# Kernel optimization log

Measured on AMD Instinct MI355X. Metric: run time of the kernel, lower is better.

## Reference

```python
import jax, jax.numpy as jnp
import numpy as np

INPUT, HIDDEN = 8, 16

def setup_inputs() -> dict:
    key = jax.random.key(0)
    ks = jax.random.split(key, 7)
    s_ih = 1.0 / np.sqrt(HIDDEN)
    x = jax.random.normal(ks[0], (8192, 512, INPUT), dtype=jnp.float32)
    W_ih = jax.random.uniform(ks[1], (HIDDEN, INPUT), jnp.float32, -s_ih, s_ih)
    W_hh = jax.random.uniform(ks[2], (HIDDEN, HIDDEN), jnp.float32, -s_ih, s_ih)
    b_ih = jax.random.uniform(ks[3], (HIDDEN,), jnp.float32, -s_ih, s_ih)
    b_hh = jax.random.uniform(ks[4], (HIDDEN,), jnp.float32, -s_ih, s_ih)
    s_fc = 1.0 / np.sqrt(HIDDEN)
    fc_w = jax.random.uniform(ks[5], (1, HIDDEN), jnp.float32, -s_fc, s_fc)
    fc_b = jax.random.uniform(ks[6], (1,), jnp.float32, -s_fc, s_fc)
    return {"x": x, "W_ih": W_ih, "W_hh": W_hh, "b_ih": b_ih, "b_hh": b_hh, "fc_w": fc_w, "fc_b": fc_b}

def reference(x, W_ih, W_hh, b_ih, b_hh, fc_w, fc_b):
    B, T, _ = x.shape
    # Precompute input projection for all timesteps: [B, T, H]
    xp = jnp.einsum('bti,hi->bth', x, W_ih) + b_ih + b_hh
    h0 = jnp.zeros((B, HIDDEN), dtype=x.dtype)

    def step(h, xt):
        h_new = jnp.tanh(xt + h @ W_hh.T)
        return h_new, None

    h_last, _ = jax.lax.scan(step, h0, jnp.swapaxes(xp, 0, 1))
    return h_last @ fc_w.T + fc_b  # [B, 1]
```

## Files before the change

kernel.cpp:

```cpp
#include <hip/hip_runtime.h>
#include <stdint.h>


#define RNN_B   8192
#define RNN_T   512
#define RNN_IN  8
#define RNN_H   16
#define TC      32
#define NE      4
#define XROW    260
#define NTILE   (RNN_T / TC)
#define BUFSZ   (NE * XROW)

#if defined(__has_builtin)
#if __has_builtin(__builtin_amdgcn_mov_dpp)
#define ROR16(x, N) ((uint32_t)__builtin_amdgcn_mov_dpp((int)(x), 0x120 + (N), 0xF, 0xF, false))
#endif
#endif
#ifndef ROR16
#define ROR16(x, N) ((uint32_t)__builtin_amdgcn_update_dpp(0, (int)(x), 0x120 + (N), 0xF, 0xF, false))
#endif

__device__ __forceinline__ void gather16(uint32_t in, uint32_t v[16]) {
    v[0]  = in;
    v[8]  = ROR16(v[0], 8);
    v[4]  = ROR16(v[0], 4);
    v[12] = ROR16(v[8], 4);
    v[2]  = ROR16(v[0], 2);
    v[6]  = ROR16(v[4], 2);
    v[10] = ROR16(v[8], 2);
    v[14] = ROR16(v[12], 2);
    v[1]  = ROR16(v[0], 1);
    v[3]  = ROR16(v[2], 1);
    v[5]  = ROR16(v[4], 1);
    v[7]  = ROR16(v[6], 1);
    v[9]  = ROR16(v[8], 1);
    v[11] = ROR16(v[10], 1);
    v[13] = ROR16(v[12], 1);
    v[15] = ROR16(v[14], 1);
}

static __device__ __forceinline__ void stage(const float* __restrict__ x,
                                             float* lds_base, int b0, int t0,
                                             int lane)
{
#pragma unroll
    for (int e = 0; e < NE; ++e) {
        const float* gp = x + ((size_t)(b0 + e) * RNN_T + t0) * RNN_IN + lane * 4;
        float* lp = lds_base + e * XROW;
        __builtin_amdgcn_global_load_lds(
            (const __attribute__((address_space(1))) uint32_t*)gp,
            (__attribute__((address_space(3))) uint32_t*)lp,
            16, 0, 0);
    }
}

__global__ __launch_bounds__(64) void rnn_valu_kernel(
    const float* __restrict__ x,
    const float* __restrict__ W_ih,
    const float* __restrict__ W_hh,
    const float* __restrict__ b_ih,
    const float* __restrict__ b_hh,
    const float* __restrict__ fc_w,
    const float* __restrict__ fc_b,
    float* __restrict__ out)
{
    __shared__ __align__(16) float xs[2 * BUFSZ];

    const int lane = (int)threadIdx.x;
    const int j    = lane & 15;
    const int g    = lane >> 4;
    const int b0   = (int)blockIdx.x * NE;
    const float C2 = 2.8853900817779268f;

    uint32_t sv[16];
    gather16((uint32_t)j, sv);

    float whh[RNN_H];
    float rsum = 0.0f;
#pragma unroll
    for (int m = 0; m < 16; ++m) {
        const float w = W_hh[j * RNN_H + (int)sv[m]];
        whh[m] = -2.0f * C2 * w;
        rsum  += w;
    }
    const float bias_l = C2 * (b_ih[j] + b_hh[j]) + C2 * rsum;

    float wih[RNN_IN];
#pragma unroll
    for (int i = 0; i < RNN_IN; i += 4) {
        const float4 w = *(const float4*)(W_ih + j * RNN_IN + i);
        wih[i] = C2 * w.x; wih[i+1] = C2 * w.y; wih[i+2] = C2 * w.z; wih[i+3] = C2 * w.w;
    }

    stage(x, xs, b0, 0, lane);
    __syncthreads();

    float rv = 0.5f;

    for (int tile = 0; tile < NTILE; ++tile) {
        const int cur = tile & 1;

        const float* xg = xs + cur * BUFSZ + g * XROW;
        float xp[TC];
#pragma unroll
        for (int tt = 0; tt < TC; ++tt) {
            const float4 xa = *(const float4*)(xg + tt * 8);
            const float4 xb = *(const float4*)(xg + tt * 8 + 4);
            float t0 = fmaf(wih[0], xa.x, bias_l);
            t0 = fmaf(wih[1], xa.y, t0);
            t0 = fmaf(wih[2], xa.z, t0);
            t0 = fmaf(wih[3], xa.w, t0);
            float t1 = wih[4] * xb.x;
            t1 = fmaf(wih[5], xb.y, t1);
            t1 = fmaf(wih[6], xb.z, t1);
            t1 = fmaf(wih[7], xb.w, t1);
            xp[tt] = t0 + t1;
        }

        if (tile + 1 < NTILE)
            stage(x, xs + (cur ^ 1) * BUFSZ, b0, (tile + 1) * TC, lane);

#pragma unroll
        for (int tt = 0; tt < TC; ++tt) {
            uint32_t v[16];
            gather16(__float_as_uint(rv), v);

            float c0 = fmaf(whh[0],  __uint_as_float(v[0]),  xp[tt]);
            c0 = fmaf(whh[8],  __uint_as_float(v[8]),  c0);
            c0 = fmaf(whh[4],  __uint_as_float(v[4]),  c0);
            c0 = fmaf(whh[2],  __uint_as_float(v[2]),  c0);

            float c1 = whh[12] * __uint_as_float(v[12]);
            c1 = fmaf(whh[6],  __uint_as_float(v[6]),  c1);
            c1 = fmaf(whh[10], __uint_as_float(v[10]), c1);
            c1 = fmaf(whh[14], __uint_as_float(v[14]), c1);

            float c2 = whh[1] * __uint_as_float(v[1]);
            c2 = fmaf(whh[3],  __uint_as_float(v[3]),  c2);
            c2 = fmaf(whh[5],  __uint_as_float(v[5]),  c2);
            c2 = fmaf(whh[7],  __uint_as_float(v[7]),  c2);

            float c3 = whh[9] * __uint_as_float(v[9]);
            c3 = fmaf(whh[11], __uint_as_float(v[11]), c3);
            c3 = fmaf(whh[13], __uint_as_float(v[13]), c3);
            c3 = fmaf(whh[15], __uint_as_float(v[15]), c3);

            const float s = (c0 + c1) + (c2 + c3);

            const float e = __builtin_amdgcn_exp2f(s);
            rv = __builtin_amdgcn_rcpf(e + 1.0f);
        }
        __syncthreads();
    }

    const float h = fmaf(-2.0f, rv, 1.0f);
    float vsum = h * fc_w[j];
    vsum += __shfl_xor(vsum, 1);
    vsum += __shfl_xor(vsum, 2);
    vsum += __shfl_xor(vsum, 4);
    vsum += __shfl_xor(vsum, 8);
    if (j == 0) out[b0 + g] = vsum + fc_b[0];
}

extern "C" void kernel_launch(void* const* d_in, const int* in_sizes, int n_in,
                              void* d_out, int out_size, void* d_ws, size_t ws_size,
                              hipStream_t stream)
{
    const float* x    = (const float*)d_in[0];
    const float* W_ih = (const float*)d_in[1];
    const float* W_hh = (const float*)d_in[2];
    const float* b_ih = (const float*)d_in[3];
    const float* b_hh = (const float*)d_in[4];
    const float* fc_w = (const float*)d_in[5];
    const float* fc_b = (const float*)d_in[6];
    float* out = (float*)d_out;

    dim3 grid(RNN_B / NE);
    dim3 block(64);
    rnn_valu_kernel<<<grid, block, 0, stream>>>(x, W_ih, W_hh, b_ih, b_hh, fc_w, fc_b, out);
}
```

Measured before the change: 256.8 us.

## Use packed fp16 dot2 with split hi/lo weights for recurrent matvec

Packs the recurrent state into fp16 pairs and computes the 16-term hidden matvec with v_dot2 instructions. Weights are split into fp16 high and low parts to keep weight precision. This roughly halves the DPP broadcast count and the number of dependent ops per timestep on the serial recurrence. The state is rounded to fp16 each step, so numerical accuracy may degrade over 512 steps.

```diff
diff --git a/kernel.cpp b/kernel.cpp
--- a/kernel.cpp
+++ b/kernel.cpp
@@ -12,6 +12,9 @@
 #define NTILE   (RNN_T / TC)
 #define BUFSZ   (NE * XROW)
 
+typedef __fp16 half2v __attribute__((ext_vector_type(2)));
+union H2U { half2v h; uint32_t u; };
+
 #if defined(__has_builtin)
 #if __has_builtin(__builtin_amdgcn_mov_dpp)
 #define ROR16(x, N) ((uint32_t)__builtin_amdgcn_mov_dpp((int)(x), 0x120 + (N), 0xF, 0xF, false))
@@ -21,23 +24,18 @@
 #define ROR16(x, N) ((uint32_t)__builtin_amdgcn_update_dpp(0, (int)(x), 0x120 + (N), 0xF, 0xF, false))
 #endif
 
-__device__ __forceinline__ void gather16(uint32_t in, uint32_t v[16]) {
-    v[0]  = in;
-    v[8]  = ROR16(v[0], 8);
-    v[4]  = ROR16(v[0], 4);
-    v[12] = ROR16(v[8], 4);
-    v[2]  = ROR16(v[0], 2);
-    v[6]  = ROR16(v[4], 2);
-    v[10] = ROR16(v[8], 2);
-    v[14] = ROR16(v[12], 2);
-    v[1]  = ROR16(v[0], 1);
-    v[3]  = ROR16(v[2], 1);
-    v[5]  = ROR16(v[4], 1);
-    v[7]  = ROR16(v[6], 1);
-    v[9]  = ROR16(v[8], 1);
-    v[11] = ROR16(v[10], 1);
-    v[13] = ROR16(v[12], 1);
-    v[15] = ROR16(v[14], 1);
+static __device__ __forceinline__ uint32_t pkh(float a, float b) {
+    H2U t; t.h = __builtin_amdgcn_cvt_pkrtz(a, b); return t.u;
+}
+
+static __device__ __forceinline__ float fdot2f(uint32_t a, uint32_t b, float c) {
+#if defined(__has_builtin) && __has_builtin(__builtin_amdgcn_fdot2)
+    H2U x, y; x.u = a; y.u = b;
+    return __builtin_amdgcn_fdot2(x.h, y.h, c, false);
+#else
+    H2U x, y; x.u = a; y.u = b;
+    return fmaf((float)x.h[0], (float)y.h[0], fmaf((float)x.h[1], (float)y.h[1], c));
+#endif
 }
 
 static __device__ __forceinline__ void stage(const float* __restrict__ x,
@@ -55,7 +53,7 @@
     }
 }
 
-__global__ __launch_bounds__(64) void rnn_valu_kernel(
+__global__ __launch_bounds__(64) void rnn_dot2_kernel(
     const float* __restrict__ x,
     const float* __restrict__ W_ih,
     const float* __restrict__ W_hh,
@@ -73,18 +71,33 @@
     const int b0   = (int)blockIdx.x * NE;
     const float C2 = 2.8853900817779268f;
 
-    uint32_t sv[16];
-    gather16((uint32_t)j, sv);
-
-    float whh[RNN_H];
-    float rsum = 0.0f;
-#pragma unroll
-    for (int m = 0; m < 16; ++m) {
-        const float w = W_hh[j * RNN_H + (int)sv[m]];
-        whh[m] = -2.0f * C2 * w;
-        rsum  += w;
-    }
-    const float bias_l = C2 * (b_ih[j] + b_hh[j]) + C2 * rsum;
+    uint32_t A[8], Bv[8];
+    {
+        const uint32_t j0 = (uint32_t)j;
+        const uint32_t j1 = ROR16(j0, 1);
+        A[0] = j0;            Bv[0] = j1;
+        A[4] = ROR16(A[0],8); Bv[4] = ROR16(Bv[0],8);
+        A[2] = ROR16(A[0],4); Bv[2] = ROR16(Bv[0],4);
+        A[6] = ROR16(A[4],4); Bv[6] = ROR16(Bv[4],4);
+        A[1] = ROR16(A[0],2); Bv[1] = ROR16(Bv[0],2);
+        A[3] = ROR16(A[2],2); Bv[3] = ROR16(Bv[2],2);
+        A[5] = ROR16(A[4],2); Bv[5] = ROR16(Bv[4],2);
+        A[7] = ROR16(A[6],2); Bv[7] = ROR16(Bv[6],2);
+    }
+
+    uint32_t wh[8], wl[8];
+    float wsum = 0.0f;
+#pragma unroll
+    for (int t = 0; t < 8; ++t) {
+        const float wa = -2.0f * C2 * W_hh[j * RNN_H + (int)A[t]];
+        const float wb = -2.0f * C2 * W_hh[j * RNN_H + (int)Bv[t]];
+        const __fp16 wah = (__fp16)wa, wbh = (__fp16)wb;
+        const __fp16 wal = (__fp16)(wa - (float)wah), wbl = (__fp16)(wb - (float)wbh);
+        H2U h1; h1.h[0] = wah; h1.h[1] = wbh; wh[t] = h1.u;
+        H2U h2; h2.h[0] = wal; h2.h[1] = wbl; wl[t] = h2.u;
+        wsum += (float)wah + (float)wal + (float)wbh + (float)wbl;
+    }
+    const float bias_l = C2 * (b_ih[j] + b_hh[j]) - 0.5f * wsum;
 
     float wih[RNN_IN];
 #pragma unroll
@@ -123,28 +136,36 @@
 
 #pragma unroll
         for (int tt = 0; tt < TC; ++tt) {
-            uint32_t v[16];
-            gather16(__float_as_uint(rv), v);
-
-            float c0 = fmaf(whh[0],  __uint_as_float(v[0]),  xp[tt]);
-            c0 = fmaf(whh[8],  __uint_as_float(v[8]),  c0);
-            c0 = fmaf(whh[4],  __uint_as_float(v[4]),  c0);
-            c0 = fmaf(whh[2],  __uint_as_float(v[2]),  c0);
-
-            float c1 = whh[12] * __uint_as_float(v[12]);
-            c1 = fmaf(whh[6],  __uint_as_float(v[6]),  c1);
-            c1 = fmaf(whh[10], __uint_as_float(v[10]), c1);
-            c1 = fmaf(whh[14], __uint_as_float(v[14]), c1);
-
-            float c2 = whh[1] * __uint_as_float(v[1]);
-            c2 = fmaf(whh[3],  __uint_as_float(v[3]),  c2);
-            c2 = fmaf(whh[5],  __uint_as_float(v[5]),  c2);
-            c2 = fmaf(whh[7],  __uint_as_float(v[7]),  c2);
-
-            float c3 = whh[9] * __uint_as_float(v[9]);
-            c3 = fmaf(whh[11], __uint_as_float(v[11]), c3);
-            c3 = fmaf(whh[13], __uint_as_float(v[13]), c3);
-            c3 = fmaf(whh[15], __uint_as_float(v[15]), c3);
+            const uint32_t rb = __float_as_uint(rv);
+            const uint32_t rn = ROR16(rb, 1);
+            const uint32_t p0 = pkh(rv, __uint_as_float(rn));
+            const uint32_t p4 = ROR16(p0, 8);
+            const uint32_t p2 = ROR16(p0, 4);
+            const uint32_t p6 = ROR16(p4, 4);
+            const uint32_t p1 = ROR16(p0, 2);
+            const uint32_t p3 = ROR16(p2, 2);
+            const uint32_t p5 = ROR16(p4, 2);
+            const uint32_t p7 = ROR16(p6, 2);
+
+            float c0 = fdot2f(wh[0], p0, xp[tt]);
+            c0 = fdot2f(wh[4], p4, c0);
+            c0 = fdot2f(wh[2], p2, c0);
+            c0 = fdot2f(wh[1], p1, c0);
+
+            float c1 = fdot2f(wh[6], p6, 0.0f);
+            c1 = fdot2f(wh[3], p3, c1);
+            c1 = fdot2f(wh[5], p5, c1);
+            c1 = fdot2f(wh[7], p7, c1);
+
+            float c2 = fdot2f(wl[0], p0, 0.0f);
+            c2 = fdot2f(wl[4], p4, c2);
+            c2 = fdot2f(wl[2], p2, c2);
+            c2 = fdot2f(wl[3], p3, c2);
+
+            float c3 = fdot2f(wl[6], p6, 0.0f);
+            c3 = fdot2f(wl[1], p1, c3);
+            c3 = fdot2f(wl[5], p5, c3);
+            c3 = fdot2f(wl[7], p7, c3);
 
             const float s = (c0 + c1) + (c2 + c3);
 
@@ -178,5 +199,5 @@
 
     dim3 grid(RNN_B / NE);
     dim3 block(64);
-    rnn_valu_kernel<<<grid, block, 0, stream>>>(x, W_ih, W_hh, b_ih, b_hh, fc_w, fc_b, out);
-}
+    rnn_dot2_kernel<<<grid, block, 0, stream>>>(x, W_ih, W_hh, b_ih, b_hh, fc_w, fc_b, out);
+}
```

After: 250.0 us. 2.6% less time.
